# Kernel optimization log

Measured on AMD Instinct MI355X. Metric: run time of the kernel, lower is better.

## Reference

```python
import jax, jax.numpy as jnp
import numpy as np


def _affine_grid(theta, H, W):
    # theta: [N,2,3]; matches torch affine_grid(align_corners=False)
    dt = theta.dtype
    xs = (2.0 * jnp.arange(W, dtype=dt) + 1.0) / W - 1.0
    ys = (2.0 * jnp.arange(H, dtype=dt) + 1.0) / H - 1.0
    gx, gy = jnp.meshgrid(xs, ys)          # [H,W] each, x varies along W
    coords = jnp.stack([gx, gy, jnp.ones_like(gx)], axis=-1)  # [H,W,3]
    return jnp.einsum('nij,hwj->nhwi', theta, coords)         # [N,H,W,2] (x,y)


def _gather(img, yc, xc):
    # img [N,C,H,W], yc/xc [N,Ho,Wo] int -> [N,C,Ho,Wo]
    return jax.vmap(lambda im, y, x: im[:, y, x])(img, yc, xc)


def _grid_sample(img, grid, mode):
    # torch grid_sample semantics: padding_mode='zeros', align_corners=False
    N, C, H, W = img.shape
    ix = ((grid[..., 0] + 1.0) * W - 1.0) / 2.0
    iy = ((grid[..., 1] + 1.0) * H - 1.0) / 2.0
    if mode == 'nearest':
        xr, yr = jnp.round(ix), jnp.round(iy)
        inb = ((xr >= 0) & (xr <= W - 1) & (yr >= 0) & (yr <= H - 1)).astype(img.dtype)
        xc = jnp.clip(xr, 0, W - 1).astype(jnp.int32)
        yc = jnp.clip(yr, 0, H - 1).astype(jnp.int32)
        return _gather(img, yc, xc) * inb[:, None]
    # bilinear
    x0, y0 = jnp.floor(ix), jnp.floor(iy)
    wx1, wy1 = ix - x0, iy - y0
    wx0, wy0 = 1.0 - wx1, 1.0 - wy1

    def corner(xf, yf, w):
        inb = ((xf >= 0) & (xf <= W - 1) & (yf >= 0) & (yf <= H - 1)).astype(img.dtype)
        xc = jnp.clip(xf, 0, W - 1).astype(jnp.int32)
        yc = jnp.clip(yf, 0, H - 1).astype(jnp.int32)
        return _gather(img, yc, xc) * (w * inb)[:, None]

    return (corner(x0, y0, wx0 * wy0) + corner(x0 + 1, y0, wx1 * wy0)
            + corner(x0, y0 + 1, wx0 * wy1) + corner(x0 + 1, y0 + 1, wx1 * wy1))


def _rot_theta(angles_flat):
    c, s = jnp.cos(angles_flat), jnp.sin(angles_flat)
    z = jnp.zeros_like(c)
    return jnp.stack([jnp.stack([c, -s, z], -1), jnp.stack([s, c, z], -1)], axis=1)  # [N,2,3]


def _scale_theta(scales_flat):
    z = jnp.zeros_like(scales_flat)
    return jnp.stack([jnp.stack([scales_flat, z, z], -1), jnp.stack([z, scales_flat, z], -1)], axis=1)


def setup_inputs() -> dict:
    key = jax.random.key(0)
    k1, k2, k3, k4, k5, k6 = jax.random.split(key, 6)
    B, K, C, H, W = 8, 32, 3, 128, 128
    ROT_RANGE, MIN_S, MAX_S = 0.5, 0.9, 1.1
    patches = jax.random.normal(k1, (B, K, C, H, W), dtype=jnp.float32)
    patch_labels = jax.random.uniform(k2, (B, K, 1, H, W), dtype=jnp.float32)
    angles = (jax.random.uniform(k3, (B, K), dtype=jnp.float32) * 2.0 - 1.0) * ROT_RANGE
    flip_h = jax.random.randint(k4, (B, K), 0, 2).astype(bool)
    flip_v = jax.random.randint(k5, (B, K), 0, 2).astype(bool)
    scales = MIN_S + (MAX_S - MIN_S) * jax.random.uniform(k6, (B, K), dtype=jnp.float32)
    return {"patches": patches, "patch_labels": patch_labels, "angles": angles,
            "flip_h": flip_h, "flip_v": flip_v, "scales": scales}


def reference(patches, patch_labels, angles, flip_h, flip_v, scales):
    B, K, C, H, W = patches.shape
    N = B * K
    # --- continuous rotation (same grid for image/bilinear and label/nearest) ---
    grid_r = _affine_grid(_rot_theta(angles.reshape(N)), H, W)
    p = _grid_sample(patches.reshape(N, C, H, W), grid_r, 'bilinear').reshape(B, K, C, H, W)
    l = _grid_sample(patch_labels.reshape(N, 1, H, W), grid_r, 'nearest').reshape(B, K, 1, H, W)
    # --- flips (horizontal flips W axis, vertical flips H axis) ---
    fh = flip_h[:, :, None, None, None]
    fv = flip_v[:, :, None, None, None]
    p = jnp.where(fh, p[..., ::-1], p)
    p = jnp.where(fv, p[..., ::-1, :], p)
    l = jnp.where(fh, l[..., ::-1], l)
    l = jnp.where(fv, l[..., ::-1, :], l)
    # --- scaling via affine grid ---
    grid_s = _affine_grid(_scale_theta(scales.reshape(N)), H, W)
    p = _grid_sample(p.reshape(N, C, H, W), grid_s, 'bilinear').reshape(B, K, C, H, W)
    l = _grid_sample(l.reshape(N, 1, H, W), grid_s, 'nearest').reshape(B, K, 1, H, W)
    return p, l
```

## Files before the change

kernel.cpp:

```cpp
#include <hip/hip_runtime.h>

#define HH 128
#define WW 128
#define HW (HH * WW)
#define BAND 16
#define TROWS 18


__device__ __forceinline__ float norm_coord(int i) {
    return __fsub_rn(__fmul_rn((float)(2 * i + 1), 0.0078125f), 1.0f);
}

__device__ __forceinline__ float pix_coord(float g) {
    float t = __fadd_rn(g, 1.0f);
    t = __fmul_rn(t, 128.0f);
    t = __fsub_rn(t, 1.0f);
    return __fmul_rn(t, 0.5f);
}

__device__ __forceinline__ int med127(int v) {
    return min(max(v, 0), 127);
}

__global__ void __launch_bounds__(1024, 8)
pa_all(const float* __restrict__ patches,
       const float* __restrict__ labels,
       const float* __restrict__ angles,
       const int* __restrict__ flip_h,
       const int* __restrict__ flip_v,
       const float* __restrict__ scales,
       float* __restrict__ out_p,
       float* __restrict__ out_l,
       int npatch_blocks) {
    __shared__ float src[HW];
    __shared__ float tile[TROWS * WW];
    __shared__ float prm[5];
    int bid = blockIdx.x;
    int tid = threadIdx.x;
    bool is_patch = bid < npatch_blocks;
    int n = is_patch ? (bid / 3) : (bid - npatch_blocks);

    if (tid == 0) {
        double a = (double)angles[n];
        prm[0] = (float)cos(a);
        prm[1] = (float)sin(a);
        prm[2] = flip_h[n] ? -1.0f : 1.0f;
        prm[3] = flip_v[n] ? -1.0f : 1.0f;
        prm[4] = scales[n];
    }
    __syncthreads();
    float c = prm[0], s = prm[1], fsx = prm[2], fsy = prm[3], sc = prm[4];

    if (is_patch) {
        int slice = bid;

        const float4* g4 = (const float4*)(patches + (size_t)slice * HW);
        float4* s4 = (float4*)src;
        #pragma unroll
        for (int i = 0; i < HW / 4 / 1024; ++i)
            s4[i * 1024 + tid] = g4[i * 1024 + tid];

        float P = c * fsx, Q = -s * fsy;
        float R = s * fsx, S = c * fsy;
        float P635 = fabsf(P) * 63.5f, R635 = fabsf(R) * 63.5f;

        int w = tid & (WW - 1);
        float wm = (float)w - 63.5f;
        int p1row = tid >> 7;

        int w2 = (tid & 63) * 2;
        int prow = tid >> 6;
        float wx0a, wx1a, wx0b, wx1b;
        int xc0a, xc1a, xc0b, xc1b;
        {
            float ixo = fmaf(sc, (float)w2 - 63.5f, 63.5f);
            float xf = floorf(ixo);
            float fx = ixo - xf;
            int xi = (int)xf;
            wx0a = ((unsigned)xi < 128u) ? (1.0f - fx) : 0.0f;
            wx1a = ((unsigned)(xi + 1) < 128u) ? fx : 0.0f;
            xc0a = med127(xi); xc1a = med127(xi + 1);
            float ixo2 = ixo + sc;
            float xf2 = floorf(ixo2);
            float fx2 = ixo2 - xf2;
            int xi2 = (int)xf2;
            wx0b = ((unsigned)xi2 < 128u) ? (1.0f - fx2) : 0.0f;
            wx1b = ((unsigned)(xi2 + 1) < 128u) ? fx2 : 0.0f;
            xc0b = med127(xi2); xc1b = med127(xi2 + 1);
        }
        __syncthreads();

        float* op = out_p + (size_t)slice * HW;

        #pragma unroll
        for (int band = 0; band < HH / BAND; ++band) {
            int r0 = band * BAND;
            float lof = floorf(fmaf(sc, (float)r0 - 63.5f, 63.5f));
            float hif = floorf(fmaf(sc, (float)(r0 + BAND - 1) - 63.5f, 63.5f)) + 1.0f;
            int lo = max((int)lof, 0);
            int hi = min((int)hif, 127);
            bool fast2 = (lof >= 0.0f) && (hif <= 127.0f);
            int nrows = hi - lo + 1;

            #pragma unroll
            for (int it = 0; it < 3; ++it) {
                int row = it * 8 + p1row;
                if (row < nrows) {
                    float hf = (float)(lo + row) - 63.5f;
                    float midx = fmaf(Q, hf, 63.5f);
                    float midy = fmaf(S, hf, 63.5f);
                    float ix = fmaf(P, wm, midx);
                    float iy = fmaf(R, wm, midy);
                    float xf = floorf(ix), yf = floorf(iy);
                    float fx = ix - xf, fy = iy - yf;
                    int xi = (int)xf, yi = (int)yf;
                    bool fast1 = (midx - P635 >= 0.25f) && (midx + P635 <= 126.75f) &&
                                 (midy - R635 >= 0.25f) && (midy + R635 <= 126.75f);
                    float o;
                    if (fast1) {
                        int b = yi * WW + xi;
                        float v00 = src[b], v10 = src[b + 1];
                        float v01 = src[b + WW], v11 = src[b + WW + 1];
                        float ra = fmaf(fx, v10 - v00, v00);
                        float rb = fmaf(fx, v11 - v01, v01);
                        o = fmaf(fy, rb - ra, ra);
                    } else {
                        float wx0 = ((unsigned)xi < 128u) ? (1.0f - fx) : 0.0f;
                        float wx1 = ((unsigned)(xi + 1) < 128u) ? fx : 0.0f;
                        float wy0 = ((unsigned)yi < 128u) ? (1.0f - fy) : 0.0f;
                        float wy1 = ((unsigned)(yi + 1) < 128u) ? fy : 0.0f;
                        int xc0 = med127(xi), xc1 = med127(xi + 1);
                        int b0 = med127(yi) * WW, b1 = med127(yi + 1) * WW;
                        float v00 = src[b0 + xc0];
                        float v10 = src[b0 + xc1];
                        float v01 = src[b1 + xc0];
                        float v11 = src[b1 + xc1];
                        float ra = fmaf(wx1, v10, wx0 * v00);
                        float rb = fmaf(wx1, v11, wx0 * v01);
                        o = fmaf(rb, wy1, ra * wy0);
                    }
                    tile[row * WW + w] = o;
                }
            }
            __syncthreads();

            {
                int h = r0 + prow;
                float iy = fmaf(sc, (float)h - 63.5f, 63.5f);
                float yf = floorf(iy);
                float fy = iy - yf;
                int yi = (int)yf;
                float ox, oy;
                if (fast2) {
                    int t0 = (yi - lo) * WW, t1 = t0 + WW;
                    float a00 = tile[t0 + xc0a], a10 = tile[t0 + xc1a];
                    float a01 = tile[t1 + xc0a], a11 = tile[t1 + xc1a];
                    float b00 = tile[t0 + xc0b], b10 = tile[t0 + xc1b];
                    float b01 = tile[t1 + xc0b], b11 = tile[t1 + xc1b];
                    float ra = fmaf(wx1a, a10, wx0a * a00);
                    float rb = fmaf(wx1a, a11, wx0a * a01);
                    ox = fmaf(fy, rb - ra, ra);
                    float rc = fmaf(wx1b, b10, wx0b * b00);
                    float rd = fmaf(wx1b, b11, wx0b * b01);
                    oy = fmaf(fy, rd - rc, rc);
                } else {
                    float wy0 = ((unsigned)yi < 128u) ? (1.0f - fy) : 0.0f;
                    float wy1 = ((unsigned)(yi + 1) < 128u) ? fy : 0.0f;
                    int t0 = (min(max(yi, lo), hi) - lo) * WW;
                    int t1 = (min(max(yi + 1, lo), hi) - lo) * WW;
                    float a00 = tile[t0 + xc0a], a10 = tile[t0 + xc1a];
                    float a01 = tile[t1 + xc0a], a11 = tile[t1 + xc1a];
                    float b00 = tile[t0 + xc0b], b10 = tile[t0 + xc1b];
                    float b01 = tile[t1 + xc0b], b11 = tile[t1 + xc1b];
                    float ra = fmaf(wx1a, a10, wx0a * a00);
                    float rb = fmaf(wx1a, a11, wx0a * a01);
                    ox = fmaf(rb, wy1, ra * wy0);
                    float rc = fmaf(wx1b, b10, wx0b * b00);
                    float rd = fmaf(wx1b, b11, wx0b * b01);
                    oy = fmaf(rd, wy1, rc * wy0);
                }
                float2 o2;
                o2.x = ox;
                o2.y = oy;
                *(float2*)&op[h * WW + w2] = o2;
            }
            __syncthreads();
        }
    } else {
        const float* lab = labels + (size_t)n * HW;
        float* ol = out_l + (size_t)n * HW;
        int w = tid & (WW - 1);

        float ix2 = pix_coord(__fmul_rn(sc, norm_coord(w)));
        float xr2 = rintf(ix2);
        bool okx2 = (xr2 >= 0.0f) && (xr2 <= 127.0f);
        int w2 = (int)xr2;
        float xw2 = okx2 ? __fmul_rn(fsx, norm_coord(w2)) : 0.0f;
        float cx = __fmul_rn(c, xw2);
        float sx = __fmul_rn(s, xw2);

        #pragma unroll 4
        for (int i = 0; i < HW / 1024; ++i) {
            int p = i * 1024 + tid;
            int h = p >> 7;
            float iy2 = pix_coord(__fmul_rn(sc, norm_coord(h)));
            float yr2 = rintf(iy2);
            float outv = 0.0f;
            if (okx2 && yr2 >= 0.0f && yr2 <= 127.0f) {
                int h2 = (int)yr2;
                float y = __fmul_rn(fsy, norm_coord(h2));
                float xr1 = rintf(pix_coord(__fmaf_rn(-s, y, cx)));
                float yr1 = rintf(pix_coord(__fmaf_rn(c, y, sx)));
                if (xr1 >= 0.0f && xr1 <= 127.0f &&
                    yr1 >= 0.0f && yr1 <= 127.0f) {
                    outv = lab[(int)yr1 * WW + (int)xr1];
                }
            }
            ol[p] = outv;
        }
    }
}

extern "C" void kernel_launch(void* const* d_in, const int* in_sizes, int n_in,
                              void* d_out, int out_size, void* d_ws, size_t ws_size,
                              hipStream_t stream) {
    const float* patches = (const float*)d_in[0];
    const float* labels  = (const float*)d_in[1];
    const float* angles  = (const float*)d_in[2];
    const int*   flip_h  = (const int*)d_in[3];
    const int*   flip_v  = (const int*)d_in[4];
    const float* scales  = (const float*)d_in[5];

    const int N = in_sizes[2];
    float* out   = (float*)d_out;
    float* out_p = out;
    float* out_l = out + (size_t)N * 3 * HW;

    int npatch_blocks = N * 3;
    int nlabel_blocks = N;
    pa_all<<<npatch_blocks + nlabel_blocks, 1024, 0, stream>>>(
        patches, labels, angles, flip_h, flip_v, scales,
        out_p, out_l, npatch_blocks);
}
```

Measured before the change: 40.58 us.

## Double-buffer row tile and overlap next band's rotation with current scaling

Shrinks the row band from 16 to 8 rows and double-buffers the shared tile. The rotation pass for band b+1 now runs in the same step as the scaling pass for band b, so each band needs one barrier instead of two. The scaling pass now computes one output pixel per thread with scalar stores, where it previously computed two per thread with float2 stores. This adds rotation-pass iterations with idle row slots and narrower stores, and it assumes the scale keeps a band's source rows within the 10-row tile.

```diff
diff --git a/kernel.cpp b/kernel.cpp
--- a/kernel.cpp
+++ b/kernel.cpp
@@ -3,8 +3,8 @@
 #define HH 128
 #define WW 128
 #define HW (HH * WW)
-#define BAND 16
-#define TROWS 18
+#define BAND 8
+#define TROWS 10
 
 
 __device__ __forceinline__ float norm_coord(int i) {
@@ -33,7 +33,7 @@
        float* __restrict__ out_l,
        int npatch_blocks) {
     __shared__ float src[HW];
-    __shared__ float tile[TROWS * WW];
+    __shared__ float tile[2][TROWS * WW];
     __shared__ float prm[5];
     int bid = blockIdx.x;
     int tid = threadIdx.x;
@@ -66,45 +66,32 @@
 
         int w = tid & (WW - 1);
         float wm = (float)w - 63.5f;
-        int p1row = tid >> 7;
-
-        int w2 = (tid & 63) * 2;
-        int prow = tid >> 6;
-        float wx0a, wx1a, wx0b, wx1b;
-        int xc0a, xc1a, xc0b, xc1b;
+        int lrow = tid >> 7;
+
+        float wx0, wx1;
+        int xc0, xc1;
         {
-            float ixo = fmaf(sc, (float)w2 - 63.5f, 63.5f);
+            float ixo = fmaf(sc, wm, 63.5f);
             float xf = floorf(ixo);
             float fx = ixo - xf;
             int xi = (int)xf;
-            wx0a = ((unsigned)xi < 128u) ? (1.0f - fx) : 0.0f;
-            wx1a = ((unsigned)(xi + 1) < 128u) ? fx : 0.0f;
-            xc0a = med127(xi); xc1a = med127(xi + 1);
-            float ixo2 = ixo + sc;
-            float xf2 = floorf(ixo2);
-            float fx2 = ixo2 - xf2;
-            int xi2 = (int)xf2;
-            wx0b = ((unsigned)xi2 < 128u) ? (1.0f - fx2) : 0.0f;
-            wx1b = ((unsigned)(xi2 + 1) < 128u) ? fx2 : 0.0f;
-            xc0b = med127(xi2); xc1b = med127(xi2 + 1);
+            wx0 = ((unsigned)xi < 128u) ? (1.0f - fx) : 0.0f;
+            wx1 = ((unsigned)(xi + 1) < 128u) ? fx : 0.0f;
+            xc0 = med127(xi); xc1 = med127(xi + 1);
         }
         __syncthreads();
 
         float* op = out_p + (size_t)slice * HW;
 
-        #pragma unroll
-        for (int band = 0; band < HH / BAND; ++band) {
-            int r0 = band * BAND;
-            float lof = floorf(fmaf(sc, (float)r0 - 63.5f, 63.5f));
-            float hif = floorf(fmaf(sc, (float)(r0 + BAND - 1) - 63.5f, 63.5f)) + 1.0f;
+        {
+            float lof = floorf(fmaf(sc, -63.5f, 63.5f));
+            float hif = floorf(fmaf(sc, 7.0f - 63.5f, 63.5f)) + 1.0f;
             int lo = max((int)lof, 0);
             int hi = min((int)hif, 127);
-            bool fast2 = (lof >= 0.0f) && (hif <= 127.0f);
             int nrows = hi - lo + 1;
-
             #pragma unroll
-            for (int it = 0; it < 3; ++it) {
-                int row = it * 8 + p1row;
+            for (int it = 0; it < 2; ++it) {
+                int row = it * 8 + lrow;
                 if (row < nrows) {
                     float hf = (float)(lo + row) - 63.5f;
                     float midx = fmaf(Q, hf, 63.5f);
@@ -125,64 +112,111 @@
                         float rb = fmaf(fx, v11 - v01, v01);
                         o = fmaf(fy, rb - ra, ra);
                     } else {
-                        float wx0 = ((unsigned)xi < 128u) ? (1.0f - fx) : 0.0f;
-                        float wx1 = ((unsigned)(xi + 1) < 128u) ? fx : 0.0f;
-                        float wy0 = ((unsigned)yi < 128u) ? (1.0f - fy) : 0.0f;
-                        float wy1 = ((unsigned)(yi + 1) < 128u) ? fy : 0.0f;
-                        int xc0 = med127(xi), xc1 = med127(xi + 1);
-                        int b0 = med127(yi) * WW, b1 = med127(yi + 1) * WW;
-                        float v00 = src[b0 + xc0];
-                        float v10 = src[b0 + xc1];
-                        float v01 = src[b1 + xc0];
-                        float v11 = src[b1 + xc1];
-                        float ra = fmaf(wx1, v10, wx0 * v00);
-                        float rb = fmaf(wx1, v11, wx0 * v01);
-                        o = fmaf(rb, wy1, ra * wy0);
+                        float a0 = ((unsigned)xi < 128u) ? (1.0f - fx) : 0.0f;
+                        float a1 = ((unsigned)(xi + 1) < 128u) ? fx : 0.0f;
+                        float b0 = ((unsigned)yi < 128u) ? (1.0f - fy) : 0.0f;
+                        float b1 = ((unsigned)(yi + 1) < 128u) ? fy : 0.0f;
+                        int q0 = med127(xi), q1 = med127(xi + 1);
+                        int p0 = med127(yi) * WW, p1 = med127(yi + 1) * WW;
+                        float v00 = src[p0 + q0];
+                        float v10 = src[p0 + q1];
+                        float v01 = src[p1 + q0];
+                        float v11 = src[p1 + q1];
+                        float ra = fmaf(a1, v10, a0 * v00);
+                        float rb = fmaf(a1, v11, a0 * v01);
+                        o = fmaf(rb, b1, ra * b0);
                     }
-                    tile[row * WW + w] = o;
-                }
-            }
-            __syncthreads();
+                    tile[0][row * WW + w] = o;
+                }
+            }
+        }
+        __syncthreads();
+
+        #pragma unroll
+        for (int band = 0; band < HH / BAND; ++band) {
+            int nb = band + 1;
+            if (nb < HH / BAND) {
+                float nlof = floorf(fmaf(sc, (float)(nb * BAND) - 63.5f, 63.5f));
+                float nhif = floorf(fmaf(sc, (float)(nb * BAND + BAND - 1) - 63.5f, 63.5f)) + 1.0f;
+                int nlo = max((int)nlof, 0);
+                int nhi = min((int)nhif, 127);
+                int nnrows = nhi - nlo + 1;
+                float* tdst = tile[nb & 1];
+                #pragma unroll
+                for (int it = 0; it < 2; ++it) {
+                    int row = it * 8 + lrow;
+                    if (row < nnrows) {
+                        float hf = (float)(nlo + row) - 63.5f;
+                        float midx = fmaf(Q, hf, 63.5f);
+                        float midy = fmaf(S, hf, 63.5f);
+                        float ix = fmaf(P, wm, midx);
+                        float iy = fmaf(R, wm, midy);
+                        float xf = floorf(ix), yf = floorf(iy);
+                        float fx = ix - xf, fy = iy - yf;
+                        int xi = (int)xf, yi = (int)yf;
+                        bool fast1 = (midx - P635 >= 0.25f) && (midx + P635 <= 126.75f) &&
+                                     (midy - R635 >= 0.25f) && (midy + R635 <= 126.75f);
+                        float o;
+                        if (fast1) {
+                            int b = yi * WW + xi;
+                            float v00 = src[b], v10 = src[b + 1];
+                            float v01 = src[b + WW], v11 = src[b + WW + 1];
+                            float ra = fmaf(fx, v10 - v00, v00);
+                            float rb = fmaf(fx, v11 - v01, v01);
+                            o = fmaf(fy, rb - ra, ra);
+                        } else {
+                            float a0 = ((unsigned)xi < 128u) ? (1.0f - fx) : 0.0f;
+                            float a1 = ((unsigned)(xi + 1) < 128u) ? fx : 0.0f;
+                            float b0 = ((unsigned)yi < 128u) ? (1.0f - fy) : 0.0f;
+                            float b1 = ((unsigned)(yi + 1) < 128u) ? fy : 0.0f;
+                            int q0 = med127(xi), q1 = med127(xi + 1);
+                            int p0 = med127(yi) * WW, p1 = med127(yi + 1) * WW;
+                            float v00 = src[p0 + q0];
+                            float v10 = src[p0 + q1];
+                            float v01 = src[p1 + q0];
+                            float v11 = src[p1 + q1];
+                            float ra = fmaf(a1, v10, a0 * v00);
+                            float rb = fmaf(a1, v11, a0 * v01);
+                            o = fmaf(rb, b1, ra * b0);
+                        }
+                        tdst[row * WW + w] = o;
+                    }
+                }
+            }
 
             {
-                int h = r0 + prow;
+                float lof = floorf(fmaf(sc, (float)(band * BAND) - 63.5f, 63.5f));
+                float hif = floorf(fmaf(sc, (float)(band * BAND + BAND - 1) - 63.5f, 63.5f)) + 1.0f;
+                int lo = max((int)lof, 0);
+                int hi = min((int)hif, 127);
+                bool fast2 = (lof >= 0.0f) && (hif <= 127.0f);
+                const float* tsrc = tile[band & 1];
+
+                int h = band * BAND + lrow;
                 float iy = fmaf(sc, (float)h - 63.5f, 63.5f);
                 float yf = floorf(iy);
                 float fy = iy - yf;
                 int yi = (int)yf;
-                float ox, oy;
+                float o;
                 if (fast2) {
                     int t0 = (yi - lo) * WW, t1 = t0 + WW;
-                    float a00 = tile[t0 + xc0a], a10 = tile[t0 + xc1a];
-                    float a01 = tile[t1 + xc0a], a11 = tile[t1 + xc1a];
-                    float b00 = tile[t0 + xc0b], b10 = tile[t0 + xc1b];
-                    float b01 = tile[t1 + xc0b], b11 = tile[t1 + xc1b];
-                    float ra = fmaf(wx1a, a10, wx0a * a00);
-                    float rb = fmaf(wx1a, a11, wx0a * a01);
-                    ox = fmaf(fy, rb - ra, ra);
-                    float rc = fmaf(wx1b, b10, wx0b * b00);
-                    float rd = fmaf(wx1b, b11, wx0b * b01);
-                    oy = fmaf(fy, rd - rc, rc);
+                    float v00 = tsrc[t0 + xc0], v10 = tsrc[t0 + xc1];
+                    float v01 = tsrc[t1 + xc0], v11 = tsrc[t1 + xc1];
+                    float ra = fmaf(wx1, v10, wx0 * v00);
+                    float rb = fmaf(wx1, v11, wx0 * v01);
+                    o = fmaf(fy, rb - ra, ra);
                 } else {
                     float wy0 = ((unsigned)yi < 128u) ? (1.0f - fy) : 0.0f;
                     float wy1 = ((unsigned)(yi + 1) < 128u) ? fy : 0.0f;
                     int t0 = (min(max(yi, lo), hi) - lo) * WW;
                     int t1 = (min(max(yi + 1, lo), hi) - lo) * WW;
-                    float a00 = tile[t0 + xc0a], a10 = tile[t0 + xc1a];
-                    float a01 = tile[t1 + xc0a], a11 = tile[t1 + xc1a];
-                    float b00 = tile[t0 + xc0b], b10 = tile[t0 + xc1b];
-                    float b01 = tile[t1 + xc0b], b11 = tile[t1 + xc1b];
-                    float ra = fmaf(wx1a, a10, wx0a * a00);
-                    float rb = fmaf(wx1a, a11, wx0a * a01);
-                    ox = fmaf(rb, wy1, ra * wy0);
-                    float rc = fmaf(wx1b, b10, wx0b * b00);
-                    float rd = fmaf(wx1b, b11, wx0b * b01);
-                    oy = fmaf(rd, wy1, rc * wy0);
-                }
-                float2 o2;
-                o2.x = ox;
-                o2.y = oy;
-                *(float2*)&op[h * WW + w2] = o2;
+                    float v00 = tsrc[t0 + xc0], v10 = tsrc[t0 + xc1];
+                    float v01 = tsrc[t1 + xc0], v11 = tsrc[t1 + xc1];
+                    float ra = fmaf(wx1, v10, wx0 * v00);
+                    float rb = fmaf(wx1, v11, wx0 * v01);
+                    o = fmaf(rb, wy1, ra * wy0);
+                }
+                op[h * WW + w] = o;
             }
             __syncthreads();
         }
```

Result: slower. 42.87 us (+5.7%).
